# Optimization experiments

Measured on AMD Instinct MI355X. Metric: run time of the kernel, lower is better.

The kernel has to match this reference:

```python
import jax, jax.numpy as jnp
import numpy as np

B, T, D, U = 64, 512, 512, 512  # units must equal input feature dim (concat along axis -2)


def setup_inputs() -> dict:
    key = jax.random.key(0)
    ks = jax.random.split(key, 5)
    glorot = float(np.sqrt(2.0 / (D + U)))  # glorot_normal std
    x = jax.random.normal(ks[0], (B, T, D), dtype=jnp.float32)
    Wq = jax.random.normal(ks[1], (D, U), dtype=jnp.float32) * glorot
    Wk = jax.random.normal(ks[2], (D, U), dtype=jnp.float32) * glorot
    Wv = jax.random.normal(ks[3], (D, U), dtype=jnp.float32) * glorot
    Wrec = jax.random.normal(ks[4], (U, U), dtype=jnp.float32) * glorot
    return {"x": x, "Wq": Wq, "Wk": Wk, "Wv": Wv, "Wrec": Wrec}


def reference(x, Wq, Wk, Wv, Wrec):
    # Self_RNN forward (inference: dropout mask == ones).
    # Recurrent step over time:
    #   hist = h @ Wrec ; inp3 = stack([hist, prev_input, x_t]) -> (B,3,D)
    #   Q,K,V = inp3 @ {Wq,Wk,Wv}                              -> (B,3,U)
    #   keras batch_dot(key^T, query, axes=[1,2]) => scores[b,i,j] = K[b,i]·Q[b,j]
    #   softmax over j (the query axis); output row i=0 only:
    #   out = sum_j softmax_j(K[b,0]·Q[b,j]/sqrt(U)) * V[b,j]
    #   new states: (out, x_t).  K.rnn -> return last output.
    units = Wq.shape[1]
    scale = 1.0 / jnp.sqrt(jnp.asarray(units, x.dtype))

    def step(carry, x_t):
        h, prev = carry
        hist = h @ Wrec                               # (B,U)
        inp3 = jnp.stack([hist, prev, x_t], axis=1)   # (B,3,D)
        Q = inp3 @ Wq                                 # (B,3,U)
        K0 = inp3[:, 0] @ Wk                          # only key row 0 (hist) is used
        V = inp3 @ Wv                                 # (B,3,U)
        scores = jnp.einsum('bu,bju->bj', K0, Q) * scale   # (B,3)
        attn = jax.nn.softmax(scores, axis=-1)
        out = jnp.einsum('bj,bju->bu', attn, V)       # (B,U)
        return (out, x_t), None

    h0 = jnp.zeros((x.shape[0], units), x.dtype)
    p0 = jnp.zeros((x.shape[0], x.shape[-1]), x.dtype)
    (h_last, _), _ = jax.lax.scan(step, (h0, p0), jnp.swapaxes(x, 0, 1))
    return h_last
```

## Files before the change

### kernel.cpp

```cpp
#include <hip/hip_runtime.h>


typedef _Float16 f16;
typedef _Float16 half8 __attribute__((ext_vector_type(8)));
typedef _Float16 h2 __attribute__((ext_vector_type(2)));
typedef float floatx4 __attribute__((ext_vector_type(4)));
typedef unsigned long long u64;

#define AM_F32 0
#define AM_F16 1
#define BM_NN_F32 0
#define BM_BT_F16 1
#define BM_BT_F32 2

#if defined(__has_builtin)
#if __has_builtin(__builtin_amdgcn_fdot2)
#define HAS_FDOT2 1
#endif
#endif

__device__ inline float dot2f(h2 a, h2 b, float c) {
#ifdef HAS_FDOT2
  return __builtin_amdgcn_fdot2(a, b, c, false);
#else
  return c + (float)a[0] * (float)b[0] + (float)a[1] * (float)b[1];
#endif
}

template<int AMODE, int BMODE, int CT>
__global__ __launch_bounds__(256)
void gemm128(const void* __restrict__ Ap, const void* __restrict__ Bp,
             f16* __restrict__ C, int K, int ldbnn, long ldc, long coff,
             int ntiles) {
  __shared__ f16 Al[128 * 32];
  __shared__ f16 Bl[128 * 32];
  const int tid = threadIdx.x;
  const int lane = tid & 63;
  const int wid = tid >> 6;
  const int wr = wid >> 1, wc = wid & 1;
  const int mt = blockIdx.x / ntiles, nt = blockIdx.x % ntiles;
  const long m0 = (long)mt * 128, n0 = (long)nt * 128;

  floatx4 acc[4][4];
#pragma unroll
  for (int m = 0; m < 4; ++m)
#pragma unroll
    for (int n = 0; n < 4; ++n) acc[m][n] = (floatx4){0.f, 0.f, 0.f, 0.f};

  for (int k0 = 0; k0 < K; k0 += 32) {
    __syncthreads();
#pragma unroll
    for (int i = 0; i < 2; ++i) {
      const int slot = i * 256 + tid;
      const int row = slot >> 2;
      const int kc = (slot & 3) * 8;
      if constexpr (AMODE == AM_F16) {
        const f16* Ag = (const f16*)Ap;
        half8 v = *(const half8*)(Ag + (m0 + row) * (long)K + k0 + kc);
        *(half8*)(Al + slot * 8) = v;
      } else {
        const float* Ag = (const float*)Ap;
        const float* p = Ag + (m0 + row) * (long)K + k0 + kc;
        float4 v0 = *(const float4*)(p);
        float4 v1 = *(const float4*)(p + 4);
        half8 h;
        h[0] = (f16)v0.x; h[1] = (f16)v0.y; h[2] = (f16)v0.z; h[3] = (f16)v0.w;
        h[4] = (f16)v1.x; h[5] = (f16)v1.y; h[6] = (f16)v1.z; h[7] = (f16)v1.w;
        *(half8*)(Al + slot * 8) = h;
      }
    }
    if constexpr (BMODE == BM_NN_F32) {
      const float* Bg = (const float*)Bp;
      const int nn = tid & 127;
      const int kh = (tid >> 7) * 16;
#pragma unroll
      for (int j = 0; j < 16; j += 2) {
        float b0 = Bg[(long)(k0 + kh + j) * ldbnn + n0 + nn];
        float b1 = Bg[(long)(k0 + kh + j + 1) * ldbnn + n0 + nn];
        h2 hv; hv[0] = (f16)b0; hv[1] = (f16)b1;
        *(h2*)(Bl + nn * 32 + kh + j) = hv;
      }
    } else {
#pragma unroll
      for (int i = 0; i < 2; ++i) {
        const int slot = i * 256 + tid;
        const int row = slot >> 2;
        const int kc = (slot & 3) * 8;
        if constexpr (BMODE == BM_BT_F16) {
          const f16* Bg = (const f16*)Bp;
          half8 v = *(const half8*)(Bg + (n0 + row) * (long)K + k0 + kc);
          *(half8*)(Bl + slot * 8) = v;
        } else {
          const float* Bg = (const float*)Bp;
          const float* p = Bg + (n0 + row) * (long)K + k0 + kc;
          float4 v0 = *(const float4*)(p);
          float4 v1 = *(const float4*)(p + 4);
          half8 h;
          h[0] = (f16)v0.x; h[1] = (f16)v0.y; h[2] = (f16)v0.z; h[3] = (f16)v0.w;
          h[4] = (f16)v1.x; h[5] = (f16)v1.y; h[6] = (f16)v1.z; h[7] = (f16)v1.w;
          *(half8*)(Bl + slot * 8) = h;
        }
      }
    }
    __syncthreads();
    const int frow = lane & 15;
    const int fkc = (lane >> 4) * 8;
    half8 af[4], bf[4];
#pragma unroll
    for (int m = 0; m < 4; ++m)
      af[m] = *(const half8*)(Al + (wr * 64 + m * 16 + frow) * 32 + fkc);
#pragma unroll
    for (int n = 0; n < 4; ++n)
      bf[n] = *(const half8*)(Bl + (wc * 64 + n * 16 + frow) * 32 + fkc);
#pragma unroll
    for (int m = 0; m < 4; ++m)
#pragma unroll
      for (int n = 0; n < 4; ++n)
        acc[m][n] = __builtin_amdgcn_mfma_f32_16x16x32_f16(af[m], bf[n],
                                                           acc[m][n], 0, 0, 0);
  }
  const int crow = (lane >> 4) * 4;
  const int ccol = lane & 15;
#pragma unroll
  for (int m = 0; m < 4; ++m)
#pragma unroll
    for (int n = 0; n < 4; ++n)
#pragma unroll
      for (int r = 0; r < 4; ++r) {
        long row = m0 + wr * 64 + m * 16 + crow + r;
        long col = n0 + wc * 64 + n * 16 + ccol;
        if constexpr (CT)
          C[(coff + col) * ldc + row] = (f16)acc[m][n][r];
        else
          C[row * ldc + coff + col] = (f16)acc[m][n][r];
      }
}

__global__ void zero_ybuf(u64* ybuf) {
  ybuf[(size_t)blockIdx.x * 256 + threadIdx.x] = 0ull;
}

__global__ __launch_bounds__(256, 1)
void seq_kernel(const f16* __restrict__ Wt, const f16* __restrict__ GXV,
                u64* __restrict__ ybuf, float* __restrict__ out) {
  const int wg = blockIdx.x;
  const int grp = wg & 15;
  const int s = wg >> 4;
  const int tid = threadIdx.x;
  const int lane = tid & 63;
  const int wid = tid >> 6;
  const int T = 512;

  __shared__ __align__(16) char wlds[64 * 1024];
  __shared__ __align__(16) char hpkb[16 * 1024];
  __shared__ float swred[4][8];
  __shared__ float aa[4][4];

  {
    const int col = tid >> 2;
    const int seg = (tid & 3) * 256;
    const unsigned key = ((unsigned)col & 7u) << 4;
    const char* src = (const char*)(Wt + (size_t)(s * 64 + col) * 512);
#pragma unroll
    for (int k = 0; k < 16; ++k) {
      half8 v = *(const half8*)(src + seg + k * 16);
      *(half8*)(wlds + col * 1024 + ((unsigned)(seg + k * 16) ^ key)) = v;
    }
  }
#pragma unroll
  for (int i = 0; i < 4; ++i)
    *(floatx4*)(hpkb + tid * 64 + i * 16) = (floatx4){0.f, 0.f, 0.f, 0.f};
  __syncthreads();

  const float scale = 0.04419417382415922f;
  const bool isV = (s < 8);
  u64* const yVp = ybuf;
  u64* const s0p = ybuf + 32768;

  const int arow = lane & 15;
  const unsigned abkey = ((unsigned)(arow & 7)) << 4;
  const int kseg = (lane >> 4) * 16;

  for (int t = 0; t < T; ++t) {
    const int par = t & 1;
    const u64 tagw = ((u64)(unsigned)(t + 1)) << 32;

    h2 xc4[4], xp4[4], gcv[4], gpv[4];
#pragma unroll
    for (int c4 = 0; c4 < 4; ++c4) {
      const f16* rowc = GXV + (((size_t)grp * 4 + c4) * T + t) * 1024;
      gcv[c4] = *(const h2*)(rowc + 2 * tid);
      xc4[c4] = *(const h2*)(rowc + 512 + 2 * tid);
      h2 z; z[0] = (f16)0.f; z[1] = (f16)0.f;
      gpv[c4] = z; xp4[c4] = z;
      if (t > 0) {
        gpv[c4] = *(const h2*)(rowc - 1024 + 2 * tid);
        xp4[c4] = *(const h2*)(rowc - 512 + 2 * tid);
      }
    }

    floatx4 acc = (floatx4){0.f, 0.f, 0.f, 0.f};
#pragma unroll
    for (int ks = 0; ks < 16; ++ks) {
      const unsigned ko = (unsigned)(ks * 64 + kseg);
      half8 av = *(const half8*)(hpkb + arow * 1024 + (ko ^ abkey));
      half8 bv = *(const half8*)(wlds + (wid * 16 + arow) * 1024 + (ko ^ abkey));
      acc = __builtin_amdgcn_mfma_f32_16x16x32_f16(av, bv, acc, 0, 0, 0);
    }

    if (isV) {
#pragma unroll
      for (int r = 0; r < 4; ++r) {
        float v = acc[r];
        float vp = __shfl_xor(v, 1);
        if (lane < 16 && !(lane & 1)) {
          h2 pk; pk[0] = (f16)v; pk[1] = (f16)vp;
          unsigned lo; __builtin_memcpy(&lo, &pk, 4);
          __hip_atomic_store(
              yVp + (((size_t)grp * 2 + par) * 4 + r) * 256 + s * 32 + wid * 8 +
                  (lane >> 1),
              tagw | (u64)lo, __ATOMIC_RELAXED, __HIP_MEMORY_SCOPE_AGENT);
        }
      }
    } else {
      float p[4];
      const int c = (s - 8) * 64 + wid * 16 + arow;
#pragma unroll
      for (int r = 0; r < 4; ++r) {
        f16 hv = *(const f16*)(hpkb + r * 1024 +
                               (((unsigned)(2 * c)) ^ (((unsigned)r) << 4)));
        p[r] = acc[r] * (float)hv;
      }
#pragma unroll
      for (int off = 32; off > 0; off >>= 1)
#pragma unroll
        for (int r = 0; r < 4; ++r) p[r] += __shfl_down(p[r], off);
      if (lane == 0) {
#pragma unroll
        for (int r = 0; r < 4; ++r)
          __hip_atomic_store(
              s0p + (((size_t)grp * 2 + par) * 4 + r) * 32 + (s - 8) * 4 + wid,
              tagw | (u64)__float_as_uint(p[r]), __ATOMIC_RELAXED,
              __HIP_MEMORY_SCOPE_AGENT);
      }
    }

    {
      float pr[8];
#pragma unroll
      for (int c4 = 0; c4 < 4; ++c4) {
        h2 hv = *(const h2*)(hpkb + c4 * 1024 +
                             (((unsigned)(4 * tid)) ^ (((unsigned)c4) << 4)));
        pr[2 * c4] = dot2f(gpv[c4], hv, 0.f);
        pr[2 * c4 + 1] = dot2f(gcv[c4], hv, 0.f);
      }
#pragma unroll
      for (int off = 32; off > 0; off >>= 1)
#pragma unroll
        for (int i = 0; i < 8; ++i) pr[i] += __shfl_down(pr[i], off);
      if (lane == 0) {
#pragma unroll
        for (int i = 0; i < 8; ++i) swred[wid][i] = pr[i];
      }
    }
    __syncthreads();

    const u64* vb = yVp + (((size_t)grp * 2 + par) * 4) * 256 + tid;
    const u64* sb = s0p + (((size_t)grp * 2 + par) * 4 + (tid >> 5)) * 32 + (tid & 31);
    u64 v0, v1, v2, v3, sw = tagw;
    for (;;) {
      v0 = __hip_atomic_load(vb, __ATOMIC_RELAXED, __HIP_MEMORY_SCOPE_AGENT);
      v1 = __hip_atomic_load(vb + 256, __ATOMIC_RELAXED, __HIP_MEMORY_SCOPE_AGENT);
      v2 = __hip_atomic_load(vb + 512, __ATOMIC_RELAXED, __HIP_MEMORY_SCOPE_AGENT);
      v3 = __hip_atomic_load(vb + 768, __ATOMIC_RELAXED, __HIP_MEMORY_SCOPE_AGENT);
      bool ok = (v0 >= tagw) & (v1 >= tagw) & (v2 >= tagw) & (v3 >= tagw);
      if (tid < 128) {
        sw = __hip_atomic_load(sb, __ATOMIC_RELAXED, __HIP_MEMORY_SCOPE_AGENT);
        ok = ok && (sw >= tagw);
      }
      if (ok) break;
      __builtin_amdgcn_s_sleep(1);
    }

    if (tid < 128) {
      float sp = __uint_as_float((unsigned)sw);
      sp += __shfl_xor(sp, 1);
      sp += __shfl_xor(sp, 2);
      sp += __shfl_xor(sp, 4);
      sp += __shfl_xor(sp, 8);
      sp += __shfl_xor(sp, 16);
      if ((tid & 31) == 0) {
        const int c4 = tid >> 5;
        const float sv0 = sp * scale;
        const float sv1 = (swred[0][2 * c4] + swred[1][2 * c4] +
                           swred[2][2 * c4] + swred[3][2 * c4]) * scale;
        const float sv2 = (swred[0][2 * c4 + 1] + swred[1][2 * c4 + 1] +
                           swred[2][2 * c4 + 1] + swred[3][2 * c4 + 1]) * scale;
        const float mx = fmaxf(sv0, fmaxf(sv1, sv2));
        const float e0 = __expf(sv0 - mx), e1 = __expf(sv1 - mx),
                    e2 = __expf(sv2 - mx);
        const float inv = 1.f / (e0 + e1 + e2);
        aa[c4][0] = e0 * inv; aa[c4][1] = e1 * inv; aa[c4][2] = e2 * inv;
      }
    }
    __syncthreads();

    {
      u64 vw[4] = {v0, v1, v2, v3};
#pragma unroll
      for (int c4 = 0; c4 < 4; ++c4) {
        const float a0 = aa[c4][0], a1 = aa[c4][1], a2 = aa[c4][2];
        unsigned lo = (unsigned)vw[c4];
        h2 vh; __builtin_memcpy(&vh, &lo, 4);
        float hn0 = a0 * (float)vh[0] + a1 * (float)xp4[c4][0] + a2 * (float)xc4[c4][0];
        float hn1 = a0 * (float)vh[1] + a1 * (float)xp4[c4][1] + a2 * (float)xc4[c4][1];
        h2 hn; hn[0] = (f16)hn0; hn[1] = (f16)hn1;
        *(h2*)(hpkb + c4 * 1024 +
               (((unsigned)(4 * tid)) ^ (((unsigned)c4) << 4))) = hn;
        if (t == T - 1 && s == 0) {
          float* ob = out + ((size_t)grp * 4 + c4) * 512 + 2 * tid;
          ob[0] = hn0; ob[1] = hn1;
        }
      }
    }
    __syncthreads();
  }
}

extern "C" void kernel_launch(void* const* d_in, const int* in_sizes, int n_in,
                              void* d_out, int out_size, void* d_ws,
                              size_t ws_size, hipStream_t stream) {
  const float* x = (const float*)d_in[0];
  const float* Wq = (const float*)d_in[1];
  const float* Wk = (const float*)d_in[2];
  const float* Wv = (const float*)d_in[3];
  const float* Wrec = (const float*)d_in[4];
  float* out = (float*)d_out;

  char* ws = (char*)d_ws;
  f16* GXV = (f16*)ws;
  f16* Wt = (f16*)(ws + 67108864);
  f16* Wrk = (f16*)(ws + 68157440);
  f16* Wrq = (f16*)(ws + 68681728);
  f16* WgT = (f16*)(ws + 69206016);
  u64* ybuf = (u64*)(ws + 68681728);

  gemm128<AM_F32, BM_NN_F32, 0><<<16, 256, 0, stream>>>(Wrec, Wk, Wrk, 512, 512, 512, 0, 4);
  gemm128<AM_F32, BM_NN_F32, 0><<<16, 256, 0, stream>>>(Wrec, Wq, Wrq, 512, 512, 512, 0, 4);
  gemm128<AM_F32, BM_NN_F32, 1><<<16, 256, 0, stream>>>(Wrec, Wv, Wt, 512, 512, 512, 0, 4);
  gemm128<AM_F16, BM_BT_F16, 1><<<16, 256, 0, stream>>>(Wrk, Wrq, Wt, 512, 0, 512, 512, 4);
  gemm128<AM_F16, BM_BT_F32, 0><<<16, 256, 0, stream>>>(Wrk, Wq, WgT, 512, 0, 512, 0, 4);
  gemm128<AM_F32, BM_BT_F16, 0><<<1024, 256, 0, stream>>>(x, WgT, GXV, 512, 0, 1024, 0, 4);
  gemm128<AM_F32, BM_NN_F32, 0><<<1024, 256, 0, stream>>>(x, Wv, GXV, 512, 512, 1024, 512, 4);

  zero_ybuf<<<144, 256, 0, stream>>>(ybuf);

  const f16* WtC = Wt; const f16* GXVC = GXV;
  void* args[] = {(void*)&WtC, (void*)&GXVC, (void*)&ybuf, (void*)&out};
  dim3 grid(256), block(256);
  if (hipLaunchCooperativeKernel((const void*)seq_kernel, grid, block, args, 0,
                                 stream) != hipSuccess) {
    seq_kernel<<<grid, block, 0, stream>>>(WtC, GXVC, ybuf, out);
  }
}
```

Before: 1.659 ms.

## Fuse two recurrence steps per grid synchronization via algebraic two-step unrolling

The persistent sequential kernel now advances two timesteps per cross-workgroup handshake instead of one, halving the number of global spin-wait barriers. It precomputes extra composed weight matrices (Wrec·Wv products and their chains with the key/query matrices) so that the second step's scores and values can be expressed as quadratic and linear combinations of quantities computed from the current state. A new precompute kernel produces per-timestep input dot products (SD). In exchange, each step does more MFMA work (128 weight rows per block, doubled LDS), polls more flags, and evaluates a more complex two-level softmax composition that may raise fp16 rounding error.

Measured after the change: 1.737 ms. +4.7%, slower.

```diff
diff --git a/kernel.cpp b/kernel.cpp
--- a/kernel.cpp
+++ b/kernel.cpp
@@ -136,123 +136,202 @@
       }
 }
 
+__global__ void sd_kernel(const f16* __restrict__ GXV, float* __restrict__ SD) {
+  const int b = blockIdx.x >> 8;
+  const int te = (blockIdx.x & 255) << 1;
+  const int tid = threadIdx.x;
+  const int lane = tid & 63, wid = tid >> 6;
+  __shared__ float red[4][4];
+  const f16* rc = GXV + ((size_t)b * 512 + te) * 1024;
+  h2 gt = *(const h2*)(rc + 2 * tid);
+  h2 g1 = *(const h2*)(rc + 1024 + 2 * tid);
+  h2 xc = *(const h2*)(rc + 512 + 2 * tid);
+  h2 xp; xp[0] = (f16)0.f; xp[1] = (f16)0.f;
+  if (te > 0) xp = *(const h2*)(rc - 1024 + 512 + 2 * tid);
+  float p0 = dot2f(xp, gt, 0.f), p1 = dot2f(xc, gt, 0.f);
+  float p2 = dot2f(xp, g1, 0.f), p3 = dot2f(xc, g1, 0.f);
+#pragma unroll
+  for (int off = 32; off > 0; off >>= 1) {
+    p0 += __shfl_down(p0, off); p1 += __shfl_down(p1, off);
+    p2 += __shfl_down(p2, off); p3 += __shfl_down(p3, off);
+  }
+  if (lane == 0) { red[wid][0] = p0; red[wid][1] = p1; red[wid][2] = p2; red[wid][3] = p3; }
+  __syncthreads();
+  if (tid < 4)
+    SD[((size_t)b * 512 + te) * 4 + tid] =
+        red[0][tid] + red[1][tid] + red[2][tid] + red[3][tid];
+}
+
 __global__ void zero_ybuf(u64* ybuf) {
   ybuf[(size_t)blockIdx.x * 256 + threadIdx.x] = 0ull;
 }
 
 __global__ __launch_bounds__(256, 1)
-void seq_kernel(const f16* __restrict__ Wt, const f16* __restrict__ GXV,
-                u64* __restrict__ ybuf, float* __restrict__ out) {
+void seq_kernel(const f16* __restrict__ Wt4, const f16* __restrict__ GXV,
+                const float* __restrict__ SD, u64* __restrict__ ybuf,
+                float* __restrict__ out) {
   const int wg = blockIdx.x;
   const int grp = wg & 15;
   const int s = wg >> 4;
   const int tid = threadIdx.x;
   const int lane = tid & 63;
   const int wid = tid >> 6;
-  const int T = 512;
-
-  __shared__ __align__(16) char wlds[64 * 1024];
-  __shared__ __align__(16) char hpkb[16 * 1024];
+  const int rowgrp = lane >> 4;
+
+  __shared__ __align__(16) char wlds[128 * 1024];
+  __shared__ __align__(16) char apkb[16 * 1024];
+  __shared__ __align__(16) floatx4 ofr4[5 * 32];
   __shared__ float swred[4][8];
-  __shared__ float aa[4][4];
+  __shared__ float sldr[48];
 
   {
-    const int col = tid >> 2;
-    const int seg = (tid & 3) * 256;
-    const unsigned key = ((unsigned)col & 7u) << 4;
-    const char* src = (const char*)(Wt + (size_t)(s * 64 + col) * 512);
-#pragma unroll
-    for (int k = 0; k < 16; ++k) {
-      half8 v = *(const half8*)(src + seg + k * 16);
-      *(half8*)(wlds + col * 1024 + ((unsigned)(seg + k * 16) ^ key)) = v;
+    const int r = tid >> 1;
+    const int lc = r & 31;
+    const int seg = (tid & 1) * 512;
+    const unsigned key = ((unsigned)(lc & 7)) << 4;
+    const f16* src = Wt4 + (((size_t)(r >> 5) * 512) + s * 32 + lc) * 512;
+#pragma unroll
+    for (int k = 0; k < 32; ++k) {
+      half8 v = *(const half8*)((const char*)src + seg + k * 16);
+      *(half8*)(wlds + r * 1024 + ((unsigned)(seg + k * 16) ^ key)) = v;
     }
   }
 #pragma unroll
   for (int i = 0; i < 4; ++i)
-    *(floatx4*)(hpkb + tid * 64 + i * 16) = (floatx4){0.f, 0.f, 0.f, 0.f};
+    *(floatx4*)(apkb + tid * 64 + i * 16) = (floatx4){0.f, 0.f, 0.f, 0.f};
   __syncthreads();
+  {
+#pragma unroll
+    for (int c4 = 0; c4 < 4; ++c4) {
+      h2 xc0 = *(const h2*)(GXV + (((size_t)(grp * 4 + c4)) * 512) * 1024 + 512 + 2 * tid);
+      *(h2*)(apkb + (8 + c4) * 1024 +
+             (((unsigned)(4 * tid)) ^ ((((unsigned)(8 + c4)) & 7) << 4))) = xc0;
+    }
+  }
+  __syncthreads();
 
   const float scale = 0.04419417382415922f;
-  const bool isV = (s < 8);
-  u64* const yVp = ybuf;
-  u64* const s0p = ybuf + 32768;
+  u64* const yVec = ybuf;
+  u64* const sblk = ybuf + 98304;
 
   const int arow = lane & 15;
   const unsigned abkey = ((unsigned)(arow & 7)) << 4;
   const int kseg = (lane >> 4) * 16;
 
-  for (int t = 0; t < T; ++t) {
-    const int par = t & 1;
-    const u64 tagw = ((u64)(unsigned)(t + 1)) << 32;
-
-    h2 xc4[4], xp4[4], gcv[4], gpv[4];
+  for (int nb = 0; nb < 256; ++nb) {
+    const int t = nb * 2;
+    const int par = nb & 1;
+    const u64 tagw = ((u64)(unsigned)(nb + 1)) << 32;
+
+    h2 gm1[4], gt[4], xv1[4], xv2[4];
 #pragma unroll
     for (int c4 = 0; c4 < 4; ++c4) {
-      const f16* rowc = GXV + (((size_t)grp * 4 + c4) * T + t) * 1024;
-      gcv[c4] = *(const h2*)(rowc + 2 * tid);
-      xc4[c4] = *(const h2*)(rowc + 512 + 2 * tid);
-      h2 z; z[0] = (f16)0.f; z[1] = (f16)0.f;
-      gpv[c4] = z; xp4[c4] = z;
-      if (t > 0) {
-        gpv[c4] = *(const h2*)(rowc - 1024 + 2 * tid);
-        xp4[c4] = *(const h2*)(rowc - 512 + 2 * tid);
-      }
-    }
-
-    floatx4 acc = (floatx4){0.f, 0.f, 0.f, 0.f};
+      const f16* rc = GXV + (((size_t)(grp * 4 + c4)) * 512 + t) * 1024;
+      gm1[c4] = *(const h2*)(rc + (t > 0 ? -1024 : 0) + 2 * tid);
+      gt[c4] = *(const h2*)(rc + 2 * tid);
+      xv1[c4] = *(const h2*)(rc + 1024 + 512 + 2 * tid);
+      xv2[c4] = *(const h2*)(rc + (t < 510 ? 2048 : 1024) + 512 + 2 * tid);
+    }
+
+    floatx4 acc[2];
+    acc[0] = (floatx4){0.f, 0.f, 0.f, 0.f};
+    acc[1] = (floatx4){0.f, 0.f, 0.f, 0.f};
 #pragma unroll
     for (int ks = 0; ks < 16; ++ks) {
       const unsigned ko = (unsigned)(ks * 64 + kseg);
-      half8 av = *(const half8*)(hpkb + arow * 1024 + (ko ^ abkey));
-      half8 bv = *(const half8*)(wlds + (wid * 16 + arow) * 1024 + (ko ^ abkey));
-      acc = __builtin_amdgcn_mfma_f32_16x16x32_f16(av, bv, acc, 0, 0, 0);
-    }
-
-    if (isV) {
-#pragma unroll
-      for (int r = 0; r < 4; ++r) {
-        float v = acc[r];
-        float vp = __shfl_xor(v, 1);
-        if (lane < 16 && !(lane & 1)) {
-          h2 pk; pk[0] = (f16)v; pk[1] = (f16)vp;
-          unsigned lo; __builtin_memcpy(&lo, &pk, 4);
-          __hip_atomic_store(
-              yVp + (((size_t)grp * 2 + par) * 4 + r) * 256 + s * 32 + wid * 8 +
-                  (lane >> 1),
-              tagw | (u64)lo, __ATOMIC_RELAXED, __HIP_MEMORY_SCOPE_AGENT);
+      half8 av = *(const half8*)(apkb + arow * 1024 + (ko ^ abkey));
+#pragma unroll
+      for (int nt = 0; nt < 2; ++nt) {
+        half8 bv = *(const half8*)(wlds + (wid * 32 + nt * 16 + arow) * 1024 + (ko ^ abkey));
+        acc[nt] = __builtin_amdgcn_mfma_f32_16x16x32_f16(av, bv, acc[nt], 0, 0, 0);
+      }
+    }
+
+    if (wid == 1 || wid == 2) {
+#pragma unroll
+      for (int r = 0; r < 4; ++r)
+#pragma unroll
+        for (int nt = 0; nt < 2; ++nt) {
+          float v = acc[nt][r];
+          float vp = __shfl_xor(v, 1);
+          int vec = (wid == 2) ? (rowgrp == 0 ? 0 : -1)
+                               : (rowgrp == 1 ? 1 : (rowgrp == 2 ? 2 : -1));
+          if (vec >= 0 && !(lane & 1)) {
+            h2 pk; pk[0] = (f16)v; pk[1] = (f16)vp;
+            unsigned lo; __builtin_memcpy(&lo, &pk, 4);
+            __hip_atomic_store(
+                yVec + ((((size_t)grp * 2 + par) * 3 + vec) * 4 + r) * 256 +
+                    s * 16 + nt * 8 + ((lane & 15) >> 1),
+                tagw | (u64)lo, __ATOMIC_RELAXED, __HIP_MEMORY_SCOPE_AGENT);
+          }
         }
-      }
-    } else {
-      float p[4];
-      const int c = (s - 8) * 64 + wid * 16 + arow;
-#pragma unroll
-      for (int r = 0; r < 4; ++r) {
-        f16 hv = *(const f16*)(hpkb + r * 1024 +
-                               (((unsigned)(2 * c)) ^ (((unsigned)r) << 4)));
-        p[r] = acc[r] * (float)hv;
-      }
-#pragma unroll
-      for (int off = 32; off > 0; off >>= 1)
-#pragma unroll
-        for (int r = 0; r < 4; ++r) p[r] += __shfl_down(p[r], off);
-      if (lane == 0) {
-#pragma unroll
-        for (int r = 0; r < 4; ++r)
-          __hip_atomic_store(
-              s0p + (((size_t)grp * 2 + par) * 4 + r) * 32 + (s - 8) * 4 + wid,
-              tagw | (u64)__float_as_uint(p[r]), __ATOMIC_RELAXED,
-              __HIP_MEMORY_SCOPE_AGENT);
-      }
+    }
+    {
+      int vec = -1;
+      if (wid == 0 && rowgrp < 3) vec = rowgrp;
+      else if (wid == 1 && rowgrp == 0) vec = 3;
+      else if (wid == 3 && rowgrp == 0) vec = 4;
+      if (vec >= 0) {
+#pragma unroll
+        for (int nt = 0; nt < 2; ++nt)
+          ofr4[vec * 32 + nt * 16 + (lane & 15)] = acc[nt];
+      }
+    }
+    __syncthreads();
+
+    if (tid < 192) {
+      const int q = tid >> 2;
+      const int type = q >> 2;
+      const int ch = q & 3;
+      const int c0 = (tid & 3) * 8;
+      const int gbase = s * 32 + c0;
+      const int avecs[12] = {0, 3, 3, 4, 4, 4, 1, 2, 1, 1, 2, 2};
+      const int av = avecs[type];
+      const float* ofr = (const float*)ofr4;
+      float bv[8];
+      if (type == 0) {
+        half8 h8 = *(const half8*)(apkb + ch * 1024 +
+                                   (((unsigned)(2 * gbase)) ^ ((unsigned)ch << 4)));
+#pragma unroll
+        for (int j = 0; j < 8; ++j) bv[j] = (float)h8[j];
+      } else if (type == 1 || type == 2) {
+        const f16* g = GXV + (((size_t)(grp * 4 + ch)) * 512 + t + (type - 1)) * 1024 + gbase;
+        half8 g8 = *(const half8*)g;
+#pragma unroll
+        for (int j = 0; j < 8; ++j) bv[j] = (float)g8[j];
+      } else if (type == 3 || type == 6 || type == 7) {
+#pragma unroll
+        for (int j = 0; j < 8; ++j) bv[j] = ofr[(3 * 32 + c0 + j) * 4 + ch];
+      } else if (type == 4 || type == 8 || type == 10) {
+        half8 h8 = *(const half8*)(apkb + (4 + ch) * 1024 +
+                                   (((unsigned)(2 * gbase)) ^ (((unsigned)(4 + ch) & 7) << 4)));
+#pragma unroll
+        for (int j = 0; j < 8; ++j) bv[j] = (float)h8[j];
+      } else {
+        half8 h8 = *(const half8*)(apkb + (8 + ch) * 1024 +
+                                   (((unsigned)(2 * gbase)) ^ (((unsigned)(8 + ch) & 7) << 4)));
+#pragma unroll
+        for (int j = 0; j < 8; ++j) bv[j] = (float)h8[j];
+      }
+      float p = 0.f;
+#pragma unroll
+      for (int j = 0; j < 8; ++j) p += ofr[(av * 32 + c0 + j) * 4 + ch] * bv[j];
+      p += __shfl_down(p, 1);
+      p += __shfl_down(p, 2);
+      if ((tid & 3) == 0)
+        __hip_atomic_store(sblk + (((size_t)grp * 2 + par) * 48 + q) * 16 + s,
+                           tagw | (u64)__float_as_uint(p), __ATOMIC_RELAXED,
+                           __HIP_MEMORY_SCOPE_AGENT);
     }
 
     {
       float pr[8];
 #pragma unroll
       for (int c4 = 0; c4 < 4; ++c4) {
-        h2 hv = *(const h2*)(hpkb + c4 * 1024 +
+        h2 hv = *(const h2*)(apkb + c4 * 1024 +
                              (((unsigned)(4 * tid)) ^ (((unsigned)c4) << 4)));
-        pr[2 * c4] = dot2f(gpv[c4], hv, 0.f);
-        pr[2 * c4 + 1] = dot2f(gcv[c4], hv, 0.f);
+        pr[2 * c4] = dot2f(gm1[c4], hv, 0.f);
+        pr[2 * c4 + 1] = dot2f(gt[c4], hv, 0.f);
       }
 #pragma unroll
       for (int off = 32; off > 0; off >>= 1)
@@ -263,64 +342,83 @@
         for (int i = 0; i < 8; ++i) swred[wid][i] = pr[i];
       }
     }
-    __syncthreads();
-
-    const u64* vb = yVp + (((size_t)grp * 2 + par) * 4) * 256 + tid;
-    const u64* sb = s0p + (((size_t)grp * 2 + par) * 4 + (tid >> 5)) * 32 + (tid & 31);
-    u64 v0, v1, v2, v3, sw = tagw;
+
+    const u64* vb = yVec + (((size_t)grp * 2 + par) * 12) * 256 + tid;
+    const u64* sb = sblk + (((size_t)grp * 2 + par) * 48 + tid) * 16;
+    u64 vv[12];
+    u64 sv[16];
     for (;;) {
-      v0 = __hip_atomic_load(vb, __ATOMIC_RELAXED, __HIP_MEMORY_SCOPE_AGENT);
-      v1 = __hip_atomic_load(vb + 256, __ATOMIC_RELAXED, __HIP_MEMORY_SCOPE_AGENT);
-      v2 = __hip_atomic_load(vb + 512, __ATOMIC_RELAXED, __HIP_MEMORY_SCOPE_AGENT);
-      v3 = __hip_atomic_load(vb + 768, __ATOMIC_RELAXED, __HIP_MEMORY_SCOPE_AGENT);
-      bool ok = (v0 >= tagw) & (v1 >= tagw) & (v2 >= tagw) & (v3 >= tagw);
-      if (tid < 128) {
-        sw = __hip_atomic_load(sb, __ATOMIC_RELAXED, __HIP_MEMORY_SCOPE_AGENT);
-        ok = ok && (sw >= tagw);
+      bool ok = true;
+#pragma unroll
+      for (int v = 0; v < 12; ++v) {
+        vv[v] = __hip_atomic_load(vb + v * 256, __ATOMIC_RELAXED,
+                                  __HIP_MEMORY_SCOPE_AGENT);
+        ok = ok && (vv[v] >= tagw);
+      }
+      if (tid < 48) {
+#pragma unroll
+        for (int i = 0; i < 16; ++i) {
+          sv[i] = __hip_atomic_load(sb + i, __ATOMIC_RELAXED,
+                                    __HIP_MEMORY_SCOPE_AGENT);
+          ok = ok && (sv[i] >= tagw);
+        }
       }
       if (ok) break;
       __builtin_amdgcn_s_sleep(1);
     }
-
-    if (tid < 128) {
-      float sp = __uint_as_float((unsigned)sw);
-      sp += __shfl_xor(sp, 1);
-      sp += __shfl_xor(sp, 2);
-      sp += __shfl_xor(sp, 4);
-      sp += __shfl_xor(sp, 8);
-      sp += __shfl_xor(sp, 16);
-      if ((tid & 31) == 0) {
-        const int c4 = tid >> 5;
-        const float sv0 = sp * scale;
-        const float sv1 = (swred[0][2 * c4] + swred[1][2 * c4] +
-                           swred[2][2 * c4] + swred[3][2 * c4]) * scale;
-        const float sv2 = (swred[0][2 * c4 + 1] + swred[1][2 * c4 + 1] +
-                           swred[2][2 * c4 + 1] + swred[3][2 * c4 + 1]) * scale;
-        const float mx = fmaxf(sv0, fmaxf(sv1, sv2));
-        const float e0 = __expf(sv0 - mx), e1 = __expf(sv1 - mx),
-                    e2 = __expf(sv2 - mx);
-        const float inv = 1.f / (e0 + e1 + e2);
-        aa[c4][0] = e0 * inv; aa[c4][1] = e1 * inv; aa[c4][2] = e2 * inv;
-      }
+    if (tid < 48) {
+      float ssum = 0.f;
+#pragma unroll
+      for (int i = 0; i < 16; ++i) ssum += __uint_as_float((unsigned)sv[i]);
+      sldr[tid] = ssum;
     }
     __syncthreads();
 
-    {
-      u64 vw[4] = {v0, v1, v2, v3};
-#pragma unroll
-      for (int c4 = 0; c4 < 4; ++c4) {
-        const float a0 = aa[c4][0], a1 = aa[c4][1], a2 = aa[c4][2];
-        unsigned lo = (unsigned)vw[c4];
-        h2 vh; __builtin_memcpy(&vh, &lo, 4);
-        float hn0 = a0 * (float)vh[0] + a1 * (float)xp4[c4][0] + a2 * (float)xc4[c4][0];
-        float hn1 = a0 * (float)vh[1] + a1 * (float)xp4[c4][1] + a2 * (float)xc4[c4][1];
-        h2 hn; hn[0] = (f16)hn0; hn[1] = (f16)hn1;
-        *(h2*)(hpkb + c4 * 1024 +
-               (((unsigned)(4 * tid)) ^ (((unsigned)c4) << 4))) = hn;
-        if (t == T - 1 && s == 0) {
-          float* ob = out + ((size_t)grp * 4 + c4) * 512 + 2 * tid;
-          ob[0] = hn0; ob[1] = hn1;
-        }
+#pragma unroll
+    for (int c4 = 0; c4 < 4; ++c4) {
+      const float sv0 = sldr[c4] * scale;
+      const float sv1 = (swred[0][2 * c4] + swred[1][2 * c4] + swred[2][2 * c4] +
+                         swred[3][2 * c4]) * scale;
+      const float sv2 = (swred[0][2 * c4 + 1] + swred[1][2 * c4 + 1] +
+                         swred[2][2 * c4 + 1] + swred[3][2 * c4 + 1]) * scale;
+      float mx = fmaxf(sv0, fmaxf(sv1, sv2));
+      float e0 = __expf(sv0 - mx), e1 = __expf(sv1 - mx), e2 = __expf(sv2 - mx);
+      float inv = 1.f / (e0 + e1 + e2);
+      const float a0 = e0 * inv, a1 = e1 * inv, a2 = e2 * inv;
+
+      const float4 sd = *(const float4*)(SD + (((size_t)(grp * 4 + c4)) * 512 + t) * 4);
+      const float s1n = (a0 * sldr[4 + c4] + a1 * sd.x + a2 * sd.y) * scale;
+      const float s2n = (a0 * sldr[8 + c4] + a1 * sd.z + a2 * sd.w) * scale;
+      const float s0n =
+          (a0 * a0 * sldr[12 + c4] + a0 * a1 * (sldr[16 + c4] + sldr[24 + c4]) +
+           a0 * a2 * (sldr[20 + c4] + sldr[28 + c4]) + a1 * a1 * sldr[32 + c4] +
+           a1 * a2 * (sldr[36 + c4] + sldr[40 + c4]) + a2 * a2 * sldr[44 + c4]) *
+          scale;
+      mx = fmaxf(s0n, fmaxf(s1n, s2n));
+      e0 = __expf(s0n - mx); e1 = __expf(s1n - mx); e2 = __expf(s2n - mx);
+      inv = 1.f / (e0 + e1 + e2);
+      const float b0 = e0 * inv, b1 = e1 * inv, b2 = e2 * inv;
+      const float cA = b0 * a0, cB = b0 * a1, cC = b0 * a2;
+
+      unsigned lo;
+      lo = (unsigned)vv[c4];      h2 y2; __builtin_memcpy(&y2, &lo, 4);
+      lo = (unsigned)vv[4 + c4];  h2 pr_; __builtin_memcpy(&pr_, &lo, 4);
+      lo = (unsigned)vv[8 + c4];  h2 cr_; __builtin_memcpy(&cr_, &lo, 4);
+      h2 xvt = *(const h2*)(apkb + (8 + c4) * 1024 +
+                            (((unsigned)(4 * tid)) ^ ((((unsigned)(8 + c4)) & 7) << 4)));
+      float hn0 = cA * (float)y2[0] + cB * (float)pr_[0] + cC * (float)cr_[0] +
+                  b1 * (float)xvt[0] + b2 * (float)xv1[c4][0];
+      float hn1 = cA * (float)y2[1] + cB * (float)pr_[1] + cC * (float)cr_[1] +
+                  b1 * (float)xvt[1] + b2 * (float)xv1[c4][1];
+      h2 hn; hn[0] = (f16)hn0; hn[1] = (f16)hn1;
+      *(h2*)(apkb + c4 * 1024 + (((unsigned)(4 * tid)) ^ (((unsigned)c4) << 4))) = hn;
+      *(h2*)(apkb + (4 + c4) * 1024 +
+             (((unsigned)(4 * tid)) ^ ((((unsigned)(4 + c4)) & 7) << 4))) = xv1[c4];
+      *(h2*)(apkb + (8 + c4) * 1024 +
+             (((unsigned)(4 * tid)) ^ ((((unsigned)(8 + c4)) & 7) << 4))) = xv2[c4];
+      if (nb == 255 && s == 0) {
+        float* ob = out + ((size_t)grp * 4 + c4) * 512 + 2 * tid;
+        ob[0] = hn0; ob[1] = hn1;
       }
     }
     __syncthreads();
@@ -339,27 +437,37 @@
 
   char* ws = (char*)d_ws;
   f16* GXV = (f16*)ws;
-  f16* Wt = (f16*)(ws + 67108864);
-  f16* Wrk = (f16*)(ws + 68157440);
-  f16* Wrq = (f16*)(ws + 68681728);
-  f16* WgT = (f16*)(ws + 69206016);
-  u64* ybuf = (u64*)(ws + 68681728);
+  f16* Wt4 = (f16*)(ws + 67108864);
+  f16* Wrk = (f16*)(ws + 69206016);
+  f16* Wrq = (f16*)(ws + 69730304);
+  f16* WrvRM = (f16*)ws;
+  f16* WgT = (f16*)(ws + 69730304);
+  float* SD = (float*)(ws + 69206016);
+  u64* ybuf = (u64*)(ws + 69730304);
+  f16* mat0 = Wt4;
+  f16* mat1 = Wt4 + 262144;
+  f16* mat2 = Wt4 + 524288;
+  f16* mat3 = Wt4 + 786432;
 
   gemm128<AM_F32, BM_NN_F32, 0><<<16, 256, 0, stream>>>(Wrec, Wk, Wrk, 512, 512, 512, 0, 4);
   gemm128<AM_F32, BM_NN_F32, 0><<<16, 256, 0, stream>>>(Wrec, Wq, Wrq, 512, 512, 512, 0, 4);
-  gemm128<AM_F32, BM_NN_F32, 1><<<16, 256, 0, stream>>>(Wrec, Wv, Wt, 512, 512, 512, 0, 4);
-  gemm128<AM_F16, BM_BT_F16, 1><<<16, 256, 0, stream>>>(Wrk, Wrq, Wt, 512, 0, 512, 512, 4);
+  gemm128<AM_F32, BM_NN_F32, 1><<<16, 256, 0, stream>>>(Wrec, Wv, mat1, 512, 512, 512, 0, 4);
+  gemm128<AM_F32, BM_NN_F32, 0><<<16, 256, 0, stream>>>(Wrec, Wv, WrvRM, 512, 512, 512, 0, 4);
+  gemm128<AM_F16, BM_BT_F16, 1><<<16, 256, 0, stream>>>(Wrk, Wrq, mat0, 512, 0, 512, 0, 4);
+  gemm128<AM_F16, BM_BT_F16, 1><<<16, 256, 0, stream>>>(WrvRM, mat1, mat2, 512, 0, 512, 0, 4);
+  gemm128<AM_F16, BM_BT_F16, 1><<<16, 256, 0, stream>>>(WrvRM, mat0, mat3, 512, 0, 512, 0, 4);
   gemm128<AM_F16, BM_BT_F32, 0><<<16, 256, 0, stream>>>(Wrk, Wq, WgT, 512, 0, 512, 0, 4);
   gemm128<AM_F32, BM_BT_F16, 0><<<1024, 256, 0, stream>>>(x, WgT, GXV, 512, 0, 1024, 0, 4);
   gemm128<AM_F32, BM_NN_F32, 0><<<1024, 256, 0, stream>>>(x, Wv, GXV, 512, 512, 1024, 512, 4);
 
-  zero_ybuf<<<144, 256, 0, stream>>>(ybuf);
-
-  const f16* WtC = Wt; const f16* GXVC = GXV;
-  void* args[] = {(void*)&WtC, (void*)&GXVC, (void*)&ybuf, (void*)&out};
+  sd_kernel<<<16384, 256, 0, stream>>>(GXV, SD);
+  zero_ybuf<<<480, 256, 0, stream>>>(ybuf);
+
+  const f16* Wt4C = Wt4; const f16* GXVC = GXV; const float* SDC = SD;
+  void* args[] = {(void*)&Wt4C, (void*)&GXVC, (void*)&SDC, (void*)&ybuf, (void*)&out};
   dim3 grid(256), block(256);
   if (hipLaunchCooperativeKernel((const void*)seq_kernel, grid, block, args, 0,
                                  stream) != hipSuccess) {
-    seq_kernel<<<grid, block, 0, stream>>>(WtC, GXVC, ybuf, out);
-  }
-}
+    seq_kernel<<<grid, block, 0, stream>>>(Wt4C, GXVC, SDC, ybuf, out);
+  }
+}
```
